# Kernel optimization log

Measured on AMD Instinct MI355X. Metric: run time of the kernel, lower is better.

The kernel has to match this reference:

```python
import jax, jax.numpy as jnp
import numpy as np

TOPK = 8

def setup_inputs() -> dict:
    key = jax.random.key(0)
    k1, k2, k3, k4 = jax.random.split(key, 4)
    B, T, D = 4, 4096, 1024
    SUB, HALF, VDIM = 512, D // 2, 128
    query = jax.random.normal(k1, (B, T, D), dtype=jnp.float32)
    codebook1 = jax.random.normal(k2, (SUB, HALF), dtype=jnp.float32) * 0.02
    codebook2 = jax.random.normal(k3, (SUB, HALF), dtype=jnp.float32) * 0.02
    values = jax.random.normal(k4, (SUB * SUB, VDIM), dtype=jnp.float32) * 0.02
    return {"query": query, "codebook1": codebook1, "codebook2": codebook2, "values": values}

def reference(query, codebook1, codebook2, values):
    B, T, D = query.shape
    sub_keys, half = codebook1.shape
    q1 = query[..., :half]
    q2 = query[..., half:2 * half]
    # [B,T,sub_keys] score matrices
    s1 = jnp.einsum('btd,kd->btk', q1, codebook1)
    s2 = jnp.einsum('btd,kd->btk', q2, codebook2)
    tk1_vals, tk1_idx = jax.lax.top_k(s1, TOPK)
    tk2_vals, tk2_idx = jax.lax.top_k(s2, TOPK)
    # cartesian combine: [B,T,TOPK,TOPK] -> [B,T,TOPK*TOPK]
    full_idx = (tk1_idx[..., :, None] * sub_keys + tk2_idx[..., None, :]).reshape(B, T, -1)
    w1 = jax.nn.softmax(tk1_vals, axis=-1)
    w2 = jax.nn.softmax(tk2_vals, axis=-1)
    weights = (w1[..., :, None] * w2[..., None, :]).reshape(B, T, -1)
    vals = values[full_idx]  # [B,T,TOPK^2,value_dim] gather
    return jnp.einsum('btk,btkv->btv', weights, vals)
```

## Files before the change

### kernel.cpp

```cpp
#include <hip/hip_runtime.h>
#include <hip/hip_bf16.h>
#include <math.h>

#define NTOK 16384
#define DDIM 1024
#define HALF 512
#define SUB  512
#define KDIM 512
#define TOPK 8
#define NCAND 16
#define VDIM 128
#define TMB 32

typedef __attribute__((ext_vector_type(8))) short bf16x8;
typedef __attribute__((ext_vector_type(4))) float f32x4;

static __device__ __forceinline__ unsigned short f2bf(float x) {
    union { float f; unsigned u; } v; v.f = x;
    unsigned r = v.u + 0x7FFF + ((v.u >> 16) & 1);
    return (unsigned short)(r >> 16);
}

static __device__ __forceinline__ void split_bf(float x, unsigned short& h, unsigned short& l) {
    h = f2bf(x);
    union { unsigned u; float f; } hv; hv.u = ((unsigned)h) << 16;
    l = f2bf(x - hv.f);
}

__global__ __launch_bounds__(256)
void cvt_bfrag(const float* __restrict__ cb1, const float* __restrict__ cb2,
               char* __restrict__ Bp)
{
    int fid  = blockIdx.x * 256 + threadIdx.x;
    int lane = fid & 63;
    int nt   = (fid >> 6) & 7;
    int kc   = (fid >> 9) & 15;
    int cq   = (fid >> 13) & 3;
    int hf   = (fid >> 15) & 1;
    const float* cb = hf ? cb2 : cb1;
    int n  = cq * 128 + nt * 16 + (lane & 15);
    int kb = kc * 32 + (lane >> 4) * 8;
    const float* src = cb + (size_t)n * KDIM + kb;
    float4 f0 = *(const float4*)src;
    float4 f1 = *(const float4*)(src + 4);
    unsigned short hh[8], ll[8];
    split_bf(f0.x, hh[0], ll[0]); split_bf(f0.y, hh[1], ll[1]);
    split_bf(f0.z, hh[2], ll[2]); split_bf(f0.w, hh[3], ll[3]);
    split_bf(f1.x, hh[4], ll[4]); split_bf(f1.y, hh[5], ll[5]);
    split_bf(f1.z, hh[6], ll[6]); split_bf(f1.w, hh[7], ll[7]);
    size_t dst = ((size_t)(hf * 4 + cq) * 128 + (kc * 8 + nt)) * 2048 + lane * 16;
    *(int4*)(Bp + dst)        = *(const int4*)hh;
    *(int4*)(Bp + dst + 1024) = *(const int4*)ll;
}

__global__ __launch_bounds__(256, 2)
void score_topk_mfma(const float* __restrict__ query,
                     const float* __restrict__ cb1f,
                     const float* __restrict__ cb2f,
                     const char* __restrict__ Bp,
                     int*   __restrict__ tk_idx,
                     float* __restrict__ tk_val)
{
    __shared__ char smem[65536];
    char* sAh = smem;
    char* sAl = smem + 32768;
    float* sS = (float*)smem;

    const int tid  = threadIdx.x;
    const int hf   = blockIdx.y;
    const int tok0 = blockIdx.x * TMB;
    const float* __restrict__ cbf = hf ? cb2f : cb1f;
    const int qoff = hf * HALF;

    const int lane = tid & 63;
    const int wid  = tid >> 6;
    const int l15  = lane & 15;
    const int lh   = lane >> 4;
    const int l7   = lane & 7;

    #pragma unroll
    for (int i = 0; i < 8; i++) {
        int c   = i * 256 + tid;
        int row = c >> 6;
        int b8  = c & 63;
        const float* src = query + (size_t)(tok0 + row) * DDIM + qoff + b8 * 8;
        float4 f0 = *(const float4*)(src);
        float4 f1 = *(const float4*)(src + 4);
        unsigned short hh[8], ll[8];
        split_bf(f0.x, hh[0], ll[0]); split_bf(f0.y, hh[1], ll[1]);
        split_bf(f0.z, hh[2], ll[2]); split_bf(f0.w, hh[3], ll[3]);
        split_bf(f1.x, hh[4], ll[4]); split_bf(f1.y, hh[5], ll[5]);
        split_bf(f1.z, hh[6], ll[6]); split_bf(f1.w, hh[7], ll[7]);
        int boff = row * 1024 + ((b8 * 16) ^ ((row & 7) << 4));
        *(int4*)(sAh + boff) = *(const int4*)hh;
        *(int4*)(sAl + boff) = *(const int4*)ll;
    }
    __syncthreads();

    const char* bp = Bp + (size_t)(hf * 4 + wid) * 262144 + lane * 16;

    int4 rh[8], rl[8];
    #pragma unroll
    for (int p = 0; p < 8; p++) {
        rh[p] = *(const int4*)(bp + p * 2048);
        rl[p] = *(const int4*)(bp + p * 2048 + 1024);
    }

    f32x4 acc[2][8];
    #pragma unroll
    for (int tg = 0; tg < 2; tg++)
        #pragma unroll
        for (int nt = 0; nt < 8; nt++) acc[tg][nt] = (f32x4){0.f, 0.f, 0.f, 0.f};

    for (int kc = 0; kc < 16; kc++) {
        const int co = (kc * 64 + lh * 16) ^ (l7 << 4);
        const bf16x8 ah0 = *(const bf16x8*)(sAh + l15 * 1024 + co);
        const bf16x8 al0 = *(const bf16x8*)(sAl + l15 * 1024 + co);
        const bf16x8 ah1 = *(const bf16x8*)(sAh + (16 + l15) * 1024 + co);
        const bf16x8 al1 = *(const bf16x8*)(sAl + (16 + l15) * 1024 + co);
        #pragma unroll
        for (int nt = 0; nt < 8; nt++) {
            union { int4 i; bf16x8 b; } ubh, ubl;
            ubh.i = rh[nt]; ubl.i = rl[nt];
            const int sp = (kc * 8 + nt + 8) & 127;
            rh[nt] = *(const int4*)(bp + sp * 2048);
            rl[nt] = *(const int4*)(bp + sp * 2048 + 1024);
            acc[0][nt] = __builtin_amdgcn_mfma_f32_16x16x32_bf16(ah0, ubh.b, acc[0][nt], 0, 0, 0);
            acc[0][nt] = __builtin_amdgcn_mfma_f32_16x16x32_bf16(al0, ubh.b, acc[0][nt], 0, 0, 0);
            acc[0][nt] = __builtin_amdgcn_mfma_f32_16x16x32_bf16(ah0, ubl.b, acc[0][nt], 0, 0, 0);
            acc[1][nt] = __builtin_amdgcn_mfma_f32_16x16x32_bf16(ah1, ubh.b, acc[1][nt], 0, 0, 0);
            acc[1][nt] = __builtin_amdgcn_mfma_f32_16x16x32_bf16(al1, ubh.b, acc[1][nt], 0, 0, 0);
            acc[1][nt] = __builtin_amdgcn_mfma_f32_16x16x32_bf16(ah1, ubl.b, acc[1][nt], 0, 0, 0);
        }
    }
    __syncthreads();

    #pragma unroll
    for (int tg = 0; tg < 2; tg++)
        #pragma unroll
        for (int nt = 0; nt < 8; nt++)
            #pragma unroll
            for (int r = 0; r < 4; r++) {
                int t = tg * 16 + lh * 4 + r;
                int c = wid * 128 + nt * 16 + l15;
                sS[t * SUB + (c ^ (lh << 3))] = acc[tg][nt][r];
            }
    __syncthreads();

    for (int v = 0; v < 8; v++) {
        const int t   = wid * 8 + v;
        const int tok = tok0 + t;
        const int hsh = ((t >> 2) & 3) << 3;

        float sv[8];
        #pragma unroll
        for (int j = 0; j < 8; j++) sv[j] = sS[t * SUB + ((lane + 64 * j) ^ hsh)];

        float m = sv[0];
        #pragma unroll
        for (int j = 1; j < 8; j++) m = fmaxf(m, sv[j]);
        #pragma unroll
        for (int off = 32; off > 0; off >>= 1) m = fmaxf(m, __shfl_xor(m, off));

        auto wave_cnt = [&](float tau) -> int {
            int c = 0;
            #pragma unroll
            for (int j = 0; j < 8; j++)
                c += __popcll(__ballot(sv[j] > tau));
            return c;
        };

        float lo = m - 0.5f, hi = m;
        while (wave_cnt(lo) < 9) lo -= 0.5f;
        for (int it = 0; it < 14; it++) {
            float mid = 0.5f * (lo + hi);
            if (wave_cnt(mid) >= 9) lo = mid; else hi = mid;
        }
        int ch8 = wave_cnt(hi);

        float v8 = 1e30f, v9 = -1e30f;
        #pragma unroll
        for (int j = 0; j < 8; j++) {
            bool sel = sv[j] > hi;
            v8 = sel ? fminf(v8, sv[j]) : v8;
            v9 = sel ? v9 : fmaxf(v9, sv[j]);
        }
        #pragma unroll
        for (int off = 32; off > 0; off >>= 1) {
            v8 = fminf(v8, __shfl_xor(v8, off));
            v9 = fmaxf(v9, __shfl_xor(v9, off));
        }

        if (ch8 == 8 && (v8 - v9) > 6e-5f) {
            int base = 0;
            #pragma unroll
            for (int j = 0; j < 8; j++) {
                unsigned long long mk = __ballot(sv[j] > hi);
                if (sv[j] > hi) {
                    int pos = base + __popcll(mk & ((1ULL << lane) - 1ULL));
                    tk_idx[((size_t)tok * 2 + hf) * TOPK + pos] = lane + 64 * j;
                    tk_val[((size_t)tok * 2 + hf) * TOPK + pos] = sv[j];
                }
                base += __popcll(mk);
            }
        } else {
            int cand[NCAND];
            #pragma unroll
            for (int r = 0; r < NCAND; r++) {
                float bv = sv[0]; int bj = 0;
                #pragma unroll
                for (int j = 1; j < 8; j++) if (sv[j] > bv) { bv = sv[j]; bj = j; }
                int bidx = lane + 64 * bj;
                #pragma unroll
                for (int off = 32; off > 0; off >>= 1) {
                    float ov = __shfl_xor(bv, off);
                    int   oi = __shfl_xor(bidx, off);
                    if (ov > bv || (ov == bv && oi < bidx)) { bv = ov; bidx = oi; }
                }
                cand[r] = bidx;
                int jj = bidx >> 6;
                if ((bidx & 63) == lane) {
                    #pragma unroll
                    for (int j = 0; j < 8; j++) if (j == jj) sv[j] = -INFINITY;
                }
            }
            double qd[8];
            #pragma unroll
            for (int j = 0; j < 8; j++)
                qd[j] = (double)query[(size_t)tok * DDIM + qoff + lane + 64 * j];
            double rv[NCAND];
            #pragma unroll
            for (int r = 0; r < NCAND; r++) {
                const float* __restrict__ crow = &cbf[(size_t)cand[r] * KDIM];
                double a = 0.0;
                #pragma unroll
                for (int j = 0; j < 8; j++)
                    a = fma(qd[j], (double)crow[lane + 64 * j], a);
                #pragma unroll
                for (int off = 32; off > 0; off >>= 1)
                    a += __shfl_xor(a, off);
                rv[r] = a;
            }
            if (lane == 0) {
                #pragma unroll
                for (int r = 0; r < NCAND; r++) {
                    int rk = 0;
                    #pragma unroll
                    for (int mm = 0; mm < NCAND; mm++)
                        if (rv[mm] > rv[r] || (rv[mm] == rv[r] && cand[mm] < cand[r])) rk++;
                    if (rk < TOPK) {
                        tk_idx[((size_t)tok * 2 + hf) * TOPK + rk] = cand[r];
                        tk_val[((size_t)tok * 2 + hf) * TOPK + rk] = (float)rv[r];
                    }
                }
            }
        }
    }
}

__global__ __launch_bounds__(256)
void gather_kernel(const float* __restrict__ values,
                   const int*   __restrict__ tk_idx,
                   const float* __restrict__ tk_val,
                   float* __restrict__ out)
{
    const int tid  = threadIdx.x;
    const int lane = tid & 63;
    const int tok  = blockIdx.x * 4 + (tid >> 6);

    const int b1 = (tok * 2 + 0) * TOPK;
    const int b2 = (tok * 2 + 1) * TOPK;

    float v1[8], v2[8]; int i1[8], i2[8];
    #pragma unroll
    for (int j = 0; j < 8; j++) {
        i1[j] = tk_idx[b1 + j]; v1[j] = tk_val[b1 + j];
        i2[j] = tk_idx[b2 + j]; v2[j] = tk_val[b2 + j];
    }

    float m1 = v1[0], m2 = v2[0];
    #pragma unroll
    for (int j = 1; j < 8; j++) { m1 = fmaxf(m1, v1[j]); m2 = fmaxf(m2, v2[j]); }

    float w1[8], w2[8], s1 = 0.f, s2 = 0.f;
    #pragma unroll
    for (int j = 0; j < 8; j++) {
        w1[j] = expf(v1[j] - m1); s1 += w1[j];
        w2[j] = expf(v2[j] - m2); s2 += w2[j];
    }
    const float inv1 = 1.f / s1, inv2 = 1.f / s2;
    #pragma unroll
    for (int j = 0; j < 8; j++) { w1[j] *= inv1; w2[j] *= inv2; }

    float2 acc = make_float2(0.f, 0.f);
    #pragma unroll
    for (int i = 0; i < 8; i++) {
        const int rb = i1[i] * SUB;
        const float wi = w1[i];
        #pragma unroll
        for (int j = 0; j < 8; j++) {
            const float w = wi * w2[j];
            const float* __restrict__ row = values + (size_t)(rb + i2[j]) * VDIM;
            float2 tv = *(const float2*)&row[lane * 2];
            acc.x = fmaf(w, tv.x, acc.x);
            acc.y = fmaf(w, tv.y, acc.y);
        }
    }
    *(float2*)&out[(size_t)tok * VDIM + lane * 2] = acc;
}

extern "C" void kernel_launch(void* const* d_in, const int* in_sizes, int n_in,
                              void* d_out, int out_size, void* d_ws, size_t ws_size,
                              hipStream_t stream) {
    const float* query  = (const float*)d_in[0];
    const float* cb1    = (const float*)d_in[1];
    const float* cb2    = (const float*)d_in[2];
    const float* values = (const float*)d_in[3];
    float* out = (float*)d_out;

    char* ws = (char*)d_ws;
    int*   tk_idx = (int*)ws;
    float* tk_val = (float*)(ws + (1u << 20));
    char*  Bp     = ws + (2u << 20);

    cvt_bfrag<<<256, 256, 0, stream>>>(cb1, cb2, Bp);
    dim3 g1(NTOK / TMB, 2);
    score_topk_mfma<<<g1, 256, 0, stream>>>(query, cb1, cb2, Bp, tk_idx, tk_val);
    gather_kernel<<<NTOK / 4, 256, 0, stream>>>(values, tk_idx, tk_val, out);
}
```

Before: 207.3 us.

## Split fused score+topk into a separate GEMM kernel and a wave-level topk kernel

When the workspace is large enough, the fused score/top-k kernel is replaced by two kernels. A 16-token-tile MFMA GEMM writes the full score matrix to global memory. A second kernel runs one wave per token-half and finds the top-8 by bisecting a threshold with ballot counts, falling back to a fp64 rescoring of 16 candidates when the cut between 8th and 9th is too tight. The gather loop also gets two accumulators for more load-level parallelism. The split trades an extra 64MB round trip of scores through memory for higher occupancy and simpler per-kernel resource use.

Result: slower. 252.6 us (+21.8%).

```diff
diff --git a/kernel.cpp b/kernel.cpp
--- a/kernel.cpp
+++ b/kernel.cpp
@@ -10,7 +10,6 @@
 #define TOPK 8
 #define NCAND 16
 #define VDIM 128
-#define TMB 32
 
 typedef __attribute__((ext_vector_type(8))) short bf16x8;
 typedef __attribute__((ext_vector_type(4))) float f32x4;
@@ -54,12 +53,221 @@
 }
 
 __global__ __launch_bounds__(256, 2)
-void score_topk_mfma(const float* __restrict__ query,
-                     const float* __restrict__ cb1f,
-                     const float* __restrict__ cb2f,
-                     const char* __restrict__ Bp,
-                     int*   __restrict__ tk_idx,
-                     float* __restrict__ tk_val)
+void score_gemm(const float* __restrict__ query,
+                const char* __restrict__ Bp,
+                float* __restrict__ scores)
+{
+    __shared__ char smem[32768];
+    char* sAh = smem;
+    char* sAl = smem + 16384;
+
+    const int tid  = threadIdx.x;
+    const int hf   = blockIdx.y;
+    const int tok0 = blockIdx.x * 16;
+    const int qoff = hf * HALF;
+
+    const int lane = tid & 63;
+    const int wid  = tid >> 6;
+    const int l15  = lane & 15;
+    const int lh   = lane >> 4;
+    const int l7   = lane & 7;
+
+    #pragma unroll
+    for (int i = 0; i < 4; i++) {
+        int c   = i * 256 + tid;
+        int row = c >> 6;
+        int b8  = c & 63;
+        const float* src = query + (size_t)(tok0 + row) * DDIM + qoff + b8 * 8;
+        float4 f0 = *(const float4*)(src);
+        float4 f1 = *(const float4*)(src + 4);
+        unsigned short hh[8], ll[8];
+        split_bf(f0.x, hh[0], ll[0]); split_bf(f0.y, hh[1], ll[1]);
+        split_bf(f0.z, hh[2], ll[2]); split_bf(f0.w, hh[3], ll[3]);
+        split_bf(f1.x, hh[4], ll[4]); split_bf(f1.y, hh[5], ll[5]);
+        split_bf(f1.z, hh[6], ll[6]); split_bf(f1.w, hh[7], ll[7]);
+        int boff = row * 1024 + ((b8 * 16) ^ ((row & 7) << 4));
+        *(int4*)(sAh + boff) = *(const int4*)hh;
+        *(int4*)(sAl + boff) = *(const int4*)ll;
+    }
+    __syncthreads();
+
+    const char* bp = Bp + (size_t)(hf * 4 + wid) * 262144 + lane * 16;
+
+    int4 rh[8], rl[8];
+    #pragma unroll
+    for (int p = 0; p < 8; p++) {
+        rh[p] = *(const int4*)(bp + p * 2048);
+        rl[p] = *(const int4*)(bp + p * 2048 + 1024);
+    }
+
+    f32x4 acc[8];
+    #pragma unroll
+    for (int nt = 0; nt < 8; nt++) acc[nt] = (f32x4){0.f, 0.f, 0.f, 0.f};
+
+    for (int kc = 0; kc < 16; kc++) {
+        const int co = (kc * 64 + lh * 16) ^ (l7 << 4);
+        const bf16x8 ah = *(const bf16x8*)(sAh + l15 * 1024 + co);
+        const bf16x8 al = *(const bf16x8*)(sAl + l15 * 1024 + co);
+        const int nb = ((kc + 1) & 15) * 8;
+
+        #pragma unroll
+        for (int nt = 0; nt < 8; nt++) {
+            union { int4 i; bf16x8 b; } u; u.i = rh[nt];
+            acc[nt] = __builtin_amdgcn_mfma_f32_16x16x32_bf16(ah, u.b, acc[nt], 0, 0, 0);
+        }
+        #pragma unroll
+        for (int nt = 0; nt < 8; nt++) {
+            union { int4 i; bf16x8 b; } u; u.i = rh[nt];
+            rh[nt] = *(const int4*)(bp + (nb + nt) * 2048);
+            acc[nt] = __builtin_amdgcn_mfma_f32_16x16x32_bf16(al, u.b, acc[nt], 0, 0, 0);
+        }
+        #pragma unroll
+        for (int nt = 0; nt < 8; nt++) {
+            union { int4 i; bf16x8 b; } u; u.i = rl[nt];
+            rl[nt] = *(const int4*)(bp + (nb + nt) * 2048 + 1024);
+            acc[nt] = __builtin_amdgcn_mfma_f32_16x16x32_bf16(ah, u.b, acc[nt], 0, 0, 0);
+        }
+    }
+
+    #pragma unroll
+    for (int nt = 0; nt < 8; nt++)
+        #pragma unroll
+        for (int r = 0; r < 4; r++) {
+            int t = tok0 + lh * 4 + r;
+            int c = hf * 512 + wid * 128 + nt * 16 + l15;
+            scores[((size_t)t << 10) + c] = acc[nt][r];
+        }
+}
+
+__global__ __launch_bounds__(256)
+void topk_kernel(const float* __restrict__ scores,
+                 const float* __restrict__ query,
+                 const float* __restrict__ cb1f,
+                 const float* __restrict__ cb2f,
+                 int*   __restrict__ tk_idx,
+                 float* __restrict__ tk_val)
+{
+    const int tid  = threadIdx.x;
+    const int lane = tid & 63;
+    const int gid  = blockIdx.x * 4 + (tid >> 6);
+    const int tok  = gid >> 1;
+    const int hf   = gid & 1;
+    const float* __restrict__ cbf = hf ? cb2f : cb1f;
+    const int qoff = hf * HALF;
+
+    float sv[8];
+    #pragma unroll
+    for (int j = 0; j < 8; j++)
+        sv[j] = scores[((size_t)tok << 10) + hf * 512 + lane + 64 * j];
+
+    float m = sv[0];
+    #pragma unroll
+    for (int j = 1; j < 8; j++) m = fmaxf(m, sv[j]);
+    #pragma unroll
+    for (int off = 32; off > 0; off >>= 1) m = fmaxf(m, __shfl_xor(m, off));
+
+    auto wave_cnt = [&](float tau) -> int {
+        int c = 0;
+        #pragma unroll
+        for (int j = 0; j < 8; j++)
+            c += __popcll(__ballot(sv[j] > tau));
+        return c;
+    };
+
+    float lo = m - 0.5f, hi = m;
+    while (wave_cnt(lo) < 9) lo -= 0.5f;
+    for (int it = 0; it < 14; it++) {
+        float mid = 0.5f * (lo + hi);
+        if (wave_cnt(mid) >= 9) lo = mid; else hi = mid;
+    }
+    int ch8 = wave_cnt(hi);
+
+    float v8 = 1e30f, v9 = -1e30f;
+    #pragma unroll
+    for (int j = 0; j < 8; j++) {
+        bool sel = sv[j] > hi;
+        v8 = sel ? fminf(v8, sv[j]) : v8;
+        v9 = sel ? v9 : fmaxf(v9, sv[j]);
+    }
+    #pragma unroll
+    for (int off = 32; off > 0; off >>= 1) {
+        v8 = fminf(v8, __shfl_xor(v8, off));
+        v9 = fmaxf(v9, __shfl_xor(v9, off));
+    }
+
+    if (ch8 == 8 && (v8 - v9) > 6e-5f) {
+        int base = 0;
+        #pragma unroll
+        for (int j = 0; j < 8; j++) {
+            unsigned long long mk = __ballot(sv[j] > hi);
+            if (sv[j] > hi) {
+                int pos = base + __popcll(mk & ((1ULL << lane) - 1ULL));
+                tk_idx[((size_t)tok * 2 + hf) * TOPK + pos] = lane + 64 * j;
+                tk_val[((size_t)tok * 2 + hf) * TOPK + pos] = sv[j];
+            }
+            base += __popcll(mk);
+        }
+    } else {
+        int cand[NCAND];
+        #pragma unroll
+        for (int r = 0; r < NCAND; r++) {
+            float bv = sv[0]; int bj = 0;
+            #pragma unroll
+            for (int j = 1; j < 8; j++) if (sv[j] > bv) { bv = sv[j]; bj = j; }
+            int bidx = lane + 64 * bj;
+            #pragma unroll
+            for (int off = 32; off > 0; off >>= 1) {
+                float ov = __shfl_xor(bv, off);
+                int   oi = __shfl_xor(bidx, off);
+                if (ov > bv || (ov == bv && oi < bidx)) { bv = ov; bidx = oi; }
+            }
+            cand[r] = bidx;
+            int jj = bidx >> 6;
+            if ((bidx & 63) == lane) {
+                #pragma unroll
+                for (int j = 0; j < 8; j++) if (j == jj) sv[j] = -INFINITY;
+            }
+        }
+        double qd[8];
+        #pragma unroll
+        for (int j = 0; j < 8; j++)
+            qd[j] = (double)query[(size_t)tok * DDIM + qoff + lane + 64 * j];
+        double rv[NCAND];
+        #pragma unroll
+        for (int r = 0; r < NCAND; r++) {
+            const float* __restrict__ crow = &cbf[(size_t)cand[r] * KDIM];
+            double a = 0.0;
+            #pragma unroll
+            for (int j = 0; j < 8; j++)
+                a = fma(qd[j], (double)crow[lane + 64 * j], a);
+            #pragma unroll
+            for (int off = 32; off > 0; off >>= 1)
+                a += __shfl_xor(a, off);
+            rv[r] = a;
+        }
+        if (lane == 0) {
+            #pragma unroll
+            for (int r = 0; r < NCAND; r++) {
+                int rk = 0;
+                #pragma unroll
+                for (int mm = 0; mm < NCAND; mm++)
+                    if (rv[mm] > rv[r] || (rv[mm] == rv[r] && cand[mm] < cand[r])) rk++;
+                if (rk < TOPK) {
+                    tk_idx[((size_t)tok * 2 + hf) * TOPK + rk] = cand[r];
+                    tk_val[((size_t)tok * 2 + hf) * TOPK + rk] = (float)rv[r];
+                }
+            }
+        }
+    }
+}
+
+__global__ __launch_bounds__(256, 2)
+void score_topk_fused(const float* __restrict__ query,
+                      const float* __restrict__ cb1f,
+                      const float* __restrict__ cb2f,
+                      const char* __restrict__ Bp,
+                      int*   __restrict__ tk_idx,
+                      float* __restrict__ tk_val)
 {
     __shared__ char smem[65536];
     char* sAh = smem;
@@ -68,7 +276,7 @@
 
     const int tid  = threadIdx.x;
     const int hf   = blockIdx.y;
-    const int tok0 = blockIdx.x * TMB;
+    const int tok0 = blockIdx.x * 32;
     const float* __restrict__ cbf = hf ? cb2f : cb1f;
     const int qoff = hf * HALF;
 
@@ -98,7 +306,6 @@
     __syncthreads();
 
     const char* bp = Bp + (size_t)(hf * 4 + wid) * 262144 + lane * 16;
-
     int4 rh[8], rl[8];
     #pragma unroll
     for (int p = 0; p < 8; p++) {
@@ -292,20 +499,26 @@
     #pragma unroll
     for (int j = 0; j < 8; j++) { w1[j] *= inv1; w2[j] *= inv2; }
 
-    float2 acc = make_float2(0.f, 0.f);
+    float2 accA = make_float2(0.f, 0.f), accB = make_float2(0.f, 0.f);
     #pragma unroll
     for (int i = 0; i < 8; i++) {
         const int rb = i1[i] * SUB;
         const float wi = w1[i];
         #pragma unroll
-        for (int j = 0; j < 8; j++) {
-            const float w = wi * w2[j];
-            const float* __restrict__ row = values + (size_t)(rb + i2[j]) * VDIM;
-            float2 tv = *(const float2*)&row[lane * 2];
-            acc.x = fmaf(w, tv.x, acc.x);
-            acc.y = fmaf(w, tv.y, acc.y);
-        }
-    }
+        for (int j = 0; j < 8; j += 2) {
+            const float wa = wi * w2[j];
+            const float wb = wi * w2[j + 1];
+            const float* __restrict__ ra = values + (size_t)(rb + i2[j])     * VDIM;
+            const float* __restrict__ rbp = values + (size_t)(rb + i2[j + 1]) * VDIM;
+            float2 ta = *(const float2*)&ra[lane * 2];
+            float2 tb = *(const float2*)&rbp[lane * 2];
+            accA.x = fmaf(wa, ta.x, accA.x);
+            accA.y = fmaf(wa, ta.y, accA.y);
+            accB.x = fmaf(wb, tb.x, accB.x);
+            accB.y = fmaf(wb, tb.y, accB.y);
+        }
+    }
+    float2 acc = make_float2(accA.x + accB.x, accA.y + accB.y);
     *(float2*)&out[(size_t)tok * VDIM + lane * 2] = acc;
 }
 
@@ -322,9 +535,18 @@
     int*   tk_idx = (int*)ws;
     float* tk_val = (float*)(ws + (1u << 20));
     char*  Bp     = ws + (2u << 20);
+    float* scores = (float*)(ws + (4u << 20));
 
     cvt_bfrag<<<256, 256, 0, stream>>>(cb1, cb2, Bp);
-    dim3 g1(NTOK / TMB, 2);
-    score_topk_mfma<<<g1, 256, 0, stream>>>(query, cb1, cb2, Bp, tk_idx, tk_val);
+
+    if (ws_size >= (68u << 20)) {
+        dim3 g1(NTOK / 16, 2);
+        score_gemm<<<g1, 256, 0, stream>>>(query, Bp, scores);
+        topk_kernel<<<NTOK * 2 / 4, 256, 0, stream>>>(scores, query, cb1, cb2,
+                                                      tk_idx, tk_val);
+    } else {
+        dim3 g1(NTOK / 32, 2);
+        score_topk_fused<<<g1, 256, 0, stream>>>(query, cb1, cb2, Bp, tk_idx, tk_val);
+    }
     gather_kernel<<<NTOK / 4, 256, 0, stream>>>(values, tk_idx, tk_val, out);
 }
```

## Enlarge score tile to 64 tokens with 8 waves and batch gather loads

Applied to the files above, without the earlier changes.

Each score block now covers 64 tokens with 512 threads. Each of the 8 waves owns 64 codebook columns and works on 4 token row-tiles, so every B fragment fetched from global memory feeds more MFMAs. Query A fragments are stored in shared memory in MFMA fragment order, which removes the XOR-swizzled reads. Top-k selection runs in two rounds over the shared score buffer. The gather kernel issues all 64 value-row loads up front into register buffers before accumulating, to expose memory parallelism. The cost is 128KB of shared memory per block, higher register pressure and possibly lower occupancy.

After: 252.3 us. 21.7% more time.

```diff
diff --git a/kernel.cpp b/kernel.cpp
--- a/kernel.cpp
+++ b/kernel.cpp
@@ -10,7 +10,7 @@
 #define TOPK 8
 #define NCAND 16
 #define VDIM 128
-#define TMB 32
+#define TMB 64
 
 typedef __attribute__((ext_vector_type(8))) short bf16x8;
 typedef __attribute__((ext_vector_type(4))) float f32x4;
@@ -33,12 +33,13 @@
 {
     int fid  = blockIdx.x * 256 + threadIdx.x;
     int lane = fid & 63;
-    int nt   = (fid >> 6) & 7;
-    int kc   = (fid >> 9) & 15;
-    int cq   = (fid >> 13) & 3;
-    int hf   = (fid >> 15) & 1;
+    int fp   = fid >> 6;
+    int nt   = fp & 3;
+    int kc   = (fp >> 2) & 15;
+    int w    = (fp >> 6) & 7;
+    int hf   = (fp >> 9) & 1;
     const float* cb = hf ? cb2 : cb1;
-    int n  = cq * 128 + nt * 16 + (lane & 15);
+    int n  = w * 64 + nt * 16 + (lane & 15);
     int kb = kc * 32 + (lane >> 4) * 8;
     const float* src = cb + (size_t)n * KDIM + kb;
     float4 f0 = *(const float4*)src;
@@ -48,22 +49,19 @@
     split_bf(f0.z, hh[2], ll[2]); split_bf(f0.w, hh[3], ll[3]);
     split_bf(f1.x, hh[4], ll[4]); split_bf(f1.y, hh[5], ll[5]);
     split_bf(f1.z, hh[6], ll[6]); split_bf(f1.w, hh[7], ll[7]);
-    size_t dst = ((size_t)(hf * 4 + cq) * 128 + (kc * 8 + nt)) * 2048 + lane * 16;
-    *(int4*)(Bp + dst)        = *(const int4*)hh;
-    *(int4*)(Bp + dst + 1024) = *(const int4*)ll;
-}
-
-__global__ __launch_bounds__(256, 2)
-void score_topk_mfma(const float* __restrict__ query,
-                     const float* __restrict__ cb1f,
-                     const float* __restrict__ cb2f,
-                     const char* __restrict__ Bp,
-                     int*   __restrict__ tk_idx,
-                     float* __restrict__ tk_val)
+    *(int4*)(Bp + (size_t)fp * 2048 + lane * 16)        = *(const int4*)hh;
+    *(int4*)(Bp + (size_t)fp * 2048 + lane * 16 + 1024) = *(const int4*)ll;
+}
+
+__global__ __launch_bounds__(512, 2)
+void score_topk_fused(const float* __restrict__ query,
+                      const float* __restrict__ cb1f,
+                      const float* __restrict__ cb2f,
+                      const char* __restrict__ Bp,
+                      int*   __restrict__ tk_idx,
+                      float* __restrict__ tk_val)
 {
-    __shared__ char smem[65536];
-    char* sAh = smem;
-    char* sAl = smem + 32768;
+    __shared__ char smem[131072];
     float* sS = (float*)smem;
 
     const int tid  = threadIdx.x;
@@ -76,185 +74,217 @@
     const int wid  = tid >> 6;
     const int l15  = lane & 15;
     const int lh   = lane >> 4;
-    const int l7   = lane & 7;
-
-    #pragma unroll
-    for (int i = 0; i < 8; i++) {
-        int c   = i * 256 + tid;
-        int row = c >> 6;
-        int b8  = c & 63;
-        const float* src = query + (size_t)(tok0 + row) * DDIM + qoff + b8 * 8;
-        float4 f0 = *(const float4*)(src);
-        float4 f1 = *(const float4*)(src + 4);
-        unsigned short hh[8], ll[8];
-        split_bf(f0.x, hh[0], ll[0]); split_bf(f0.y, hh[1], ll[1]);
-        split_bf(f0.z, hh[2], ll[2]); split_bf(f0.w, hh[3], ll[3]);
-        split_bf(f1.x, hh[4], ll[4]); split_bf(f1.y, hh[5], ll[5]);
-        split_bf(f1.z, hh[6], ll[6]); split_bf(f1.w, hh[7], ll[7]);
-        int boff = row * 1024 + ((b8 * 16) ^ ((row & 7) << 4));
-        *(int4*)(sAh + boff) = *(const int4*)hh;
-        *(int4*)(sAl + boff) = *(const int4*)ll;
+
+    {
+        const int tok = tid >> 3;
+        const int ks  = tid & 7;
+        const int tr  = tok >> 4;
+        const int lb  = tok & 15;
+        const float* qrow = query + (size_t)(tok0 + tok) * DDIM + qoff;
+        #pragma unroll
+        for (int it = 0; it < 4; it++) {
+            const int k = ks * 64 + it * 16;
+            float4 f0 = *(const float4*)(qrow + k);
+            float4 f1 = *(const float4*)(qrow + k + 4);
+            float4 f2 = *(const float4*)(qrow + k + 8);
+            float4 f3 = *(const float4*)(qrow + k + 12);
+            unsigned short hh[16], ll[16];
+            split_bf(f0.x, hh[0],  ll[0]);  split_bf(f0.y, hh[1],  ll[1]);
+            split_bf(f0.z, hh[2],  ll[2]);  split_bf(f0.w, hh[3],  ll[3]);
+            split_bf(f1.x, hh[4],  ll[4]);  split_bf(f1.y, hh[5],  ll[5]);
+            split_bf(f1.z, hh[6],  ll[6]);  split_bf(f1.w, hh[7],  ll[7]);
+            split_bf(f2.x, hh[8],  ll[8]);  split_bf(f2.y, hh[9],  ll[9]);
+            split_bf(f2.z, hh[10], ll[10]); split_bf(f2.w, hh[11], ll[11]);
+            split_bf(f3.x, hh[12], ll[12]); split_bf(f3.y, hh[13], ll[13]);
+            split_bf(f3.z, hh[14], ll[14]); split_bf(f3.w, hh[15], ll[15]);
+            const int kc  = k >> 5;
+            const int lw0 = lb + ((k & 31) >> 3) * 16;
+            char* base = smem + kc * 8192 + tr * 2048;
+            *(int4*)(base + lw0 * 16)              = *(const int4*)(hh);
+            *(int4*)(base + lw0 * 16 + 256)        = *(const int4*)(hh + 8);
+            *(int4*)(base + 1024 + lw0 * 16)       = *(const int4*)(ll);
+            *(int4*)(base + 1024 + lw0 * 16 + 256) = *(const int4*)(ll + 8);
+        }
     }
     __syncthreads();
 
-    const char* bp = Bp + (size_t)(hf * 4 + wid) * 262144 + lane * 16;
-
-    int4 rh[8], rl[8];
-    #pragma unroll
-    for (int p = 0; p < 8; p++) {
-        rh[p] = *(const int4*)(bp + p * 2048);
-        rl[p] = *(const int4*)(bp + p * 2048 + 1024);
-    }
-
-    f32x4 acc[2][8];
-    #pragma unroll
-    for (int tg = 0; tg < 2; tg++)
-        #pragma unroll
-        for (int nt = 0; nt < 8; nt++) acc[tg][nt] = (f32x4){0.f, 0.f, 0.f, 0.f};
+    const char* bp = Bp + (size_t)(hf * 8 + wid) * 131072 + lane * 16;
+
+    int4 ring[8];
+    #pragma unroll
+    for (int nt = 0; nt < 4; nt++) {
+        ring[nt * 2]     = *(const int4*)(bp + nt * 2048);
+        ring[nt * 2 + 1] = *(const int4*)(bp + nt * 2048 + 1024);
+    }
+
+    f32x4 acc[4][4];
+    #pragma unroll
+    for (int tr = 0; tr < 4; tr++)
+        #pragma unroll
+        for (int nt = 0; nt < 4; nt++) acc[tr][nt] = (f32x4){0.f, 0.f, 0.f, 0.f};
 
     for (int kc = 0; kc < 16; kc++) {
-        const int co = (kc * 64 + lh * 16) ^ (l7 << 4);
-        const bf16x8 ah0 = *(const bf16x8*)(sAh + l15 * 1024 + co);
-        const bf16x8 al0 = *(const bf16x8*)(sAl + l15 * 1024 + co);
-        const bf16x8 ah1 = *(const bf16x8*)(sAh + (16 + l15) * 1024 + co);
-        const bf16x8 al1 = *(const bf16x8*)(sAl + (16 + l15) * 1024 + co);
-        #pragma unroll
-        for (int nt = 0; nt < 8; nt++) {
-            union { int4 i; bf16x8 b; } ubh, ubl;
-            ubh.i = rh[nt]; ubl.i = rl[nt];
-            const int sp = (kc * 8 + nt + 8) & 127;
-            rh[nt] = *(const int4*)(bp + sp * 2048);
-            rl[nt] = *(const int4*)(bp + sp * 2048 + 1024);
-            acc[0][nt] = __builtin_amdgcn_mfma_f32_16x16x32_bf16(ah0, ubh.b, acc[0][nt], 0, 0, 0);
-            acc[0][nt] = __builtin_amdgcn_mfma_f32_16x16x32_bf16(al0, ubh.b, acc[0][nt], 0, 0, 0);
-            acc[0][nt] = __builtin_amdgcn_mfma_f32_16x16x32_bf16(ah0, ubl.b, acc[0][nt], 0, 0, 0);
-            acc[1][nt] = __builtin_amdgcn_mfma_f32_16x16x32_bf16(ah1, ubh.b, acc[1][nt], 0, 0, 0);
-            acc[1][nt] = __builtin_amdgcn_mfma_f32_16x16x32_bf16(al1, ubh.b, acc[1][nt], 0, 0, 0);
-            acc[1][nt] = __builtin_amdgcn_mfma_f32_16x16x32_bf16(ah1, ubl.b, acc[1][nt], 0, 0, 0);
+        bf16x8 ah[4], al[4];
+        #pragma unroll
+        for (int tr = 0; tr < 4; tr++) {
+            ah[tr] = *(const bf16x8*)(smem + kc * 8192 + tr * 2048 + lane * 16);
+            al[tr] = *(const bf16x8*)(smem + kc * 8192 + tr * 2048 + 1024 + lane * 16);
         }
+        const int nb = ((kc + 1) & 15) * 4;
+        #pragma unroll
+        for (int ntp = 0; ntp < 4; ntp += 2) {
+            union { int4 i; bf16x8 b; } b0h, b1h, b0l, b1l;
+            b0h.i = ring[ntp * 2];     b0l.i = ring[ntp * 2 + 1];
+            b1h.i = ring[ntp * 2 + 2]; b1l.i = ring[ntp * 2 + 3];
+            #pragma unroll
+            for (int tr = 0; tr < 4; tr++)
+                acc[tr][ntp]   = __builtin_amdgcn_mfma_f32_16x16x32_bf16(ah[tr], b0h.b, acc[tr][ntp],   0, 0, 0);
+            #pragma unroll
+            for (int tr = 0; tr < 4; tr++)
+                acc[tr][ntp+1] = __builtin_amdgcn_mfma_f32_16x16x32_bf16(ah[tr], b1h.b, acc[tr][ntp+1], 0, 0, 0);
+            ring[ntp * 2]     = *(const int4*)(bp + (nb + ntp) * 2048);
+            ring[ntp * 2 + 2] = *(const int4*)(bp + (nb + ntp + 1) * 2048);
+            #pragma unroll
+            for (int tr = 0; tr < 4; tr++)
+                acc[tr][ntp]   = __builtin_amdgcn_mfma_f32_16x16x32_bf16(al[tr], b0h.b, acc[tr][ntp],   0, 0, 0);
+            #pragma unroll
+            for (int tr = 0; tr < 4; tr++)
+                acc[tr][ntp+1] = __builtin_amdgcn_mfma_f32_16x16x32_bf16(al[tr], b1h.b, acc[tr][ntp+1], 0, 0, 0);
+            ring[ntp * 2 + 1] = *(const int4*)(bp + (nb + ntp) * 2048 + 1024);
+            ring[ntp * 2 + 3] = *(const int4*)(bp + (nb + ntp + 1) * 2048 + 1024);
+            #pragma unroll
+            for (int tr = 0; tr < 4; tr++)
+                acc[tr][ntp]   = __builtin_amdgcn_mfma_f32_16x16x32_bf16(ah[tr], b0l.b, acc[tr][ntp],   0, 0, 0);
+            #pragma unroll
+            for (int tr = 0; tr < 4; tr++)
+                acc[tr][ntp+1] = __builtin_amdgcn_mfma_f32_16x16x32_bf16(ah[tr], b1l.b, acc[tr][ntp+1], 0, 0, 0);
+        }
     }
     __syncthreads();
 
-    #pragma unroll
-    for (int tg = 0; tg < 2; tg++)
-        #pragma unroll
-        for (int nt = 0; nt < 8; nt++)
-            #pragma unroll
-            for (int r = 0; r < 4; r++) {
-                int t = tg * 16 + lh * 4 + r;
-                int c = wid * 128 + nt * 16 + l15;
-                sS[t * SUB + (c ^ (lh << 3))] = acc[tg][nt][r];
+    for (int round = 0; round < 2; round++) {
+        #pragma unroll
+        for (int tr2 = 0; tr2 < 2; tr2++)
+            #pragma unroll
+            for (int nt = 0; nt < 4; nt++)
+                #pragma unroll
+                for (int r = 0; r < 4; r++) {
+                    int t = tr2 * 16 + lh * 4 + r;
+                    int c = wid * 64 + nt * 16 + l15;
+                    sS[t * SUB + (c ^ (lh << 3))] = acc[round * 2 + tr2][nt][r];
+                }
+        __syncthreads();
+
+        for (int v = 0; v < 4; v++) {
+            const int t   = wid * 4 + v;
+            const int tok = tok0 + round * 32 + t;
+            const int hsh = ((t >> 2) & 3) << 3;
+
+            float sv[8];
+            #pragma unroll
+            for (int j = 0; j < 8; j++) sv[j] = sS[t * SUB + ((lane + 64 * j) ^ hsh)];
+
+            float m = sv[0];
+            #pragma unroll
+            for (int j = 1; j < 8; j++) m = fmaxf(m, sv[j]);
+            #pragma unroll
+            for (int off = 32; off > 0; off >>= 1) m = fmaxf(m, __shfl_xor(m, off));
+
+            auto wave_cnt = [&](float tau) -> int {
+                int c = 0;
+                #pragma unroll
+                for (int j = 0; j < 8; j++)
+                    c += __popcll(__ballot(sv[j] > tau));
+                return c;
+            };
+
+            float lo = m - 0.5f, hi = m;
+            while (wave_cnt(lo) < 9) lo -= 0.5f;
+            for (int it = 0; it < 14; it++) {
+                float mid = 0.5f * (lo + hi);
+                if (wave_cnt(mid) >= 9) lo = mid; else hi = mid;
             }
-    __syncthreads();
-
-    for (int v = 0; v < 8; v++) {
-        const int t   = wid * 8 + v;
-        const int tok = tok0 + t;
-        const int hsh = ((t >> 2) & 3) << 3;
-
-        float sv[8];
-        #pragma unroll
-        for (int j = 0; j < 8; j++) sv[j] = sS[t * SUB + ((lane + 64 * j) ^ hsh)];
-
-        float m = sv[0];
-        #pragma unroll
-        for (int j = 1; j < 8; j++) m = fmaxf(m, sv[j]);
-        #pragma unroll
-        for (int off = 32; off > 0; off >>= 1) m = fmaxf(m, __shfl_xor(m, off));
-
-        auto wave_cnt = [&](float tau) -> int {
-            int c = 0;
-            #pragma unroll
-            for (int j = 0; j < 8; j++)
-                c += __popcll(__ballot(sv[j] > tau));
-            return c;
-        };
-
-        float lo = m - 0.5f, hi = m;
-        while (wave_cnt(lo) < 9) lo -= 0.5f;
-        for (int it = 0; it < 14; it++) {
-            float mid = 0.5f * (lo + hi);
-            if (wave_cnt(mid) >= 9) lo = mid; else hi = mid;
-        }
-        int ch8 = wave_cnt(hi);
-
-        float v8 = 1e30f, v9 = -1e30f;
-        #pragma unroll
-        for (int j = 0; j < 8; j++) {
-            bool sel = sv[j] > hi;
-            v8 = sel ? fminf(v8, sv[j]) : v8;
-            v9 = sel ? v9 : fmaxf(v9, sv[j]);
-        }
-        #pragma unroll
-        for (int off = 32; off > 0; off >>= 1) {
-            v8 = fminf(v8, __shfl_xor(v8, off));
-            v9 = fmaxf(v9, __shfl_xor(v9, off));
-        }
-
-        if (ch8 == 8 && (v8 - v9) > 6e-5f) {
-            int base = 0;
+            int ch8 = wave_cnt(hi);
+
+            float v8 = 1e30f, v9 = -1e30f;
             #pragma unroll
             for (int j = 0; j < 8; j++) {
-                unsigned long long mk = __ballot(sv[j] > hi);
-                if (sv[j] > hi) {
-                    int pos = base + __popcll(mk & ((1ULL << lane) - 1ULL));
-                    tk_idx[((size_t)tok * 2 + hf) * TOPK + pos] = lane + 64 * j;
-                    tk_val[((size_t)tok * 2 + hf) * TOPK + pos] = sv[j];
-                }
-                base += __popcll(mk);
+                bool sel = sv[j] > hi;
+                v8 = sel ? fminf(v8, sv[j]) : v8;
+                v9 = sel ? v9 : fmaxf(v9, sv[j]);
             }
-        } else {
-            int cand[NCAND];
-            #pragma unroll
-            for (int r = 0; r < NCAND; r++) {
-                float bv = sv[0]; int bj = 0;
-                #pragma unroll
-                for (int j = 1; j < 8; j++) if (sv[j] > bv) { bv = sv[j]; bj = j; }
-                int bidx = lane + 64 * bj;
-                #pragma unroll
-                for (int off = 32; off > 0; off >>= 1) {
-                    float ov = __shfl_xor(bv, off);
-                    int   oi = __shfl_xor(bidx, off);
-                    if (ov > bv || (ov == bv && oi < bidx)) { bv = ov; bidx = oi; }
-                }
-                cand[r] = bidx;
-                int jj = bidx >> 6;
-                if ((bidx & 63) == lane) {
-                    #pragma unroll
-                    for (int j = 0; j < 8; j++) if (j == jj) sv[j] = -INFINITY;
-                }
+            #pragma unroll
+            for (int off = 32; off > 0; off >>= 1) {
+                v8 = fminf(v8, __shfl_xor(v8, off));
+                v9 = fmaxf(v9, __shfl_xor(v9, off));
             }
-            double qd[8];
-            #pragma unroll
-            for (int j = 0; j < 8; j++)
-                qd[j] = (double)query[(size_t)tok * DDIM + qoff + lane + 64 * j];
-            double rv[NCAND];
-            #pragma unroll
-            for (int r = 0; r < NCAND; r++) {
-                const float* __restrict__ crow = &cbf[(size_t)cand[r] * KDIM];
-                double a = 0.0;
+
+            if (ch8 == 8 && (v8 - v9) > 6e-5f) {
+                int base = 0;
+                #pragma unroll
+                for (int j = 0; j < 8; j++) {
+                    unsigned long long mk = __ballot(sv[j] > hi);
+                    if (sv[j] > hi) {
+                        int pos = base + __popcll(mk & ((1ULL << lane) - 1ULL));
+                        tk_idx[((size_t)tok * 2 + hf) * TOPK + pos] = lane + 64 * j;
+                        tk_val[((size_t)tok * 2 + hf) * TOPK + pos] = sv[j];
+                    }
+                    base += __popcll(mk);
+                }
+            } else {
+                int cand[NCAND];
+                #pragma unroll
+                for (int r = 0; r < NCAND; r++) {
+                    float bv = sv[0]; int bj = 0;
+                    #pragma unroll
+                    for (int j = 1; j < 8; j++) if (sv[j] > bv) { bv = sv[j]; bj = j; }
+                    int bidx = lane + 64 * bj;
+                    #pragma unroll
+                    for (int off = 32; off > 0; off >>= 1) {
+                        float ov = __shfl_xor(bv, off);
+                        int   oi = __shfl_xor(bidx, off);
+                        if (ov > bv || (ov == bv && oi < bidx)) { bv = ov; bidx = oi; }
+                    }
+                    cand[r] = bidx;
+                    int jj = bidx >> 6;
+                    if ((bidx & 63) == lane) {
+                        #pragma unroll
+                        for (int j = 0; j < 8; j++) if (j == jj) sv[j] = -INFINITY;
+                    }
+                }
+                double qd[8];
                 #pragma unroll
                 for (int j = 0; j < 8; j++)
-                    a = fma(qd[j], (double)crow[lane + 64 * j], a);
-                #pragma unroll
-                for (int off = 32; off > 0; off >>= 1)
-                    a += __shfl_xor(a, off);
-                rv[r] = a;
-            }
-            if (lane == 0) {
+                    qd[j] = (double)query[(size_t)tok * DDIM + qoff + lane + 64 * j];
+                double rv[NCAND];
                 #pragma unroll
                 for (int r = 0; r < NCAND; r++) {
-                    int rk = 0;
-                    #pragma unroll
-                    for (int mm = 0; mm < NCAND; mm++)
-                        if (rv[mm] > rv[r] || (rv[mm] == rv[r] && cand[mm] < cand[r])) rk++;
-                    if (rk < TOPK) {
-                        tk_idx[((size_t)tok * 2 + hf) * TOPK + rk] = cand[r];
-                        tk_val[((size_t)tok * 2 + hf) * TOPK + rk] = (float)rv[r];
+                    const float* __restrict__ crow = &cbf[(size_t)cand[r] * KDIM];
+                    double a = 0.0;
+                    #pragma unroll
+                    for (int j = 0; j < 8; j++)
+                        a = fma(qd[j], (double)crow[lane + 64 * j], a);
+                    #pragma unroll
+                    for (int off = 32; off > 0; off >>= 1)
+                        a += __shfl_xor(a, off);
+                    rv[r] = a;
+                }
+                if (lane == 0) {
+                    #pragma unroll
+                    for (int r = 0; r < NCAND; r++) {
+                        int rk = 0;
+                        #pragma unroll
+                        for (int mm = 0; mm < NCAND; mm++)
+                            if (rv[mm] > rv[r] || (rv[mm] == rv[r] && cand[mm] < cand[r])) rk++;
+                        if (rk < TOPK) {
+                            tk_idx[((size_t)tok * 2 + hf) * TOPK + rk] = cand[r];
+                            tk_val[((size_t)tok * 2 + hf) * TOPK + rk] = (float)rv[r];
+                        }
                     }
                 }
             }
         }
+        __syncthreads();
     }
 }
 
@@ -292,20 +322,32 @@
     #pragma unroll
     for (int j = 0; j < 8; j++) { w1[j] *= inv1; w2[j] *= inv2; }
 
-    float2 acc = make_float2(0.f, 0.f);
-    #pragma unroll
-    for (int i = 0; i < 8; i++) {
-        const int rb = i1[i] * SUB;
-        const float wi = w1[i];
-        #pragma unroll
-        for (int j = 0; j < 8; j++) {
-            const float w = wi * w2[j];
-            const float* __restrict__ row = values + (size_t)(rb + i2[j]) * VDIM;
-            float2 tv = *(const float2*)&row[lane * 2];
-            acc.x = fmaf(w, tv.x, acc.x);
-            acc.y = fmaf(w, tv.y, acc.y);
-        }
-    }
+    float2 bufA[32], bufB[32];
+    #pragma unroll
+    for (int k = 0; k < 32; k++) {
+        const int i = k >> 3, j = k & 7;
+        bufA[k] = *(const float2*)(values + (size_t)(i1[i] * SUB + i2[j]) * VDIM + lane * 2);
+    }
+    #pragma unroll
+    for (int k = 0; k < 32; k++) {
+        const int i = 4 + (k >> 3), j = k & 7;
+        bufB[k] = *(const float2*)(values + (size_t)(i1[i] * SUB + i2[j]) * VDIM + lane * 2);
+    }
+
+    float2 aA = make_float2(0.f, 0.f), aB = make_float2(0.f, 0.f);
+    #pragma unroll
+    for (int k = 0; k < 32; k++) {
+        const float wa = w1[k >> 3] * w2[k & 7];
+        aA.x = fmaf(wa, bufA[k].x, aA.x);
+        aA.y = fmaf(wa, bufA[k].y, aA.y);
+    }
+    #pragma unroll
+    for (int k = 0; k < 32; k++) {
+        const float wb = w1[4 + (k >> 3)] * w2[k & 7];
+        aB.x = fmaf(wb, bufB[k].x, aB.x);
+        aB.y = fmaf(wb, bufB[k].y, aB.y);
+    }
+    float2 acc = make_float2(aA.x + aB.x, aA.y + aB.y);
     *(float2*)&out[(size_t)tok * VDIM + lane * 2] = acc;
 }
 
@@ -325,6 +367,6 @@
 
     cvt_bfrag<<<256, 256, 0, stream>>>(cb1, cb2, Bp);
     dim3 g1(NTOK / TMB, 2);
-    score_topk_mfma<<<g1, 256, 0, stream>>>(query, cb1, cb2, Bp, tk_idx, tk_val);
+    score_topk_fused<<<g1, 512, 0, stream>>>(query, cb1, cb2, Bp, tk_idx, tk_val);
     gather_kernel<<<NTOK / 4, 256, 0, stream>>>(values, tk_idx, tk_val, out);
 }
```
